# Kernel tuning notes

Hardware: AMD Instinct MI355X
Metric: run time of the kernel (lower is better)

Reference implementation:

```python
import jax, jax.numpy as jnp
import numpy as np

SLOPE = 10.0
NTR = 4.0
DTR = 0.0
DELTA = 3
MARG = 2


def _gt(x):
    return jax.nn.sigmoid(x * SLOPE)


def setup_inputs() -> dict:
    key = jax.random.key(0)
    x = jax.random.uniform(key, (16, 3, 512, 512), dtype=jnp.float32)
    return {"x": x}


def reference(x):
    B, C, H, W = x.shape
    d = DELTA
    # zero-pad H and W by delta (matches the two torch.cat calls)
    im_b = jnp.pad(x, ((0, 0), (0, 0), (d, d), (d, d)))

    roll_hw = lambda s: jnp.roll(im_b, s, axis=(2, 3))
    diff_11 = roll_hw((1, 1)) - im_b
    diff_nn11 = roll_hw((-1, -1)) - im_b
    diff_01 = roll_hw((0, 1)) - im_b
    diff_n01 = roll_hw((0, -1)) - im_b
    diff_10 = roll_hw((1, 0)) - im_b
    diff_n10 = roll_hw((-1, 0)) - im_b
    diff_n11 = roll_hw((-1, 1)) - im_b
    diff_1n1 = roll_hw((1, -1)) - im_b

    # NOTE: the original rolls the diff tensors over dims (1,2) = (channel, H).
    # We reproduce that exactly for faithfulness.
    rl = lambda t, s: jnp.roll(t, s, axis=(1, 2))

    ad_10 = jnp.abs(diff_10)
    ad_10 = ad_10 * _gt(ad_10 - DTR)
    e10a = _gt(ad_10 - jnp.abs(diff_01)) + _gt(ad_10 - jnp.abs(diff_n01)) + _gt(ad_10 - jnp.abs(diff_n10))
    # original repeats the roll(diff_01) term twice
    e10b = (_gt(ad_10 - jnp.abs(rl(diff_01, (1, 0))))
            + _gt(ad_10 - jnp.abs(rl(diff_n01, (1, 0))))
            + _gt(ad_10 - jnp.abs(rl(diff_01, (1, 0)))))
    g10 = _gt(e10a + e10b - NTR)
    e10 = g10 * _gt(diff_10)
    e10n = g10 * _gt(-diff_10)

    ad_01 = jnp.abs(diff_01)
    ad_01 = ad_01 * _gt(ad_10 - DTR)  # original uses ad_10 here (faithful)
    e01a = _gt(ad_01 - jnp.abs(diff_10)) + _gt(ad_01 - jnp.abs(diff_n10)) + _gt(ad_01 - jnp.abs(diff_n01))
    e01b = (_gt(ad_01 - jnp.abs(rl(diff_10, (0, 1))))
            + _gt(ad_01 - jnp.abs(rl(diff_n10, (0, 1))))
            + _gt(ad_01 - jnp.abs(rl(diff_01, (0, 1)))))
    g01 = _gt(e01a + e01b - NTR)
    e01 = g01 * _gt(diff_01)
    e01n = g01 * _gt(diff_01)  # original uses +diff_01 for both (faithful)

    ad_11 = jnp.abs(diff_11)
    ad_11 = ad_11 * _gt(ad_11 - DTR)
    e11a = _gt(ad_11 - jnp.abs(diff_n11)) + _gt(ad_11 - jnp.abs(diff_1n1)) + _gt(ad_11 - jnp.abs(diff_nn11))
    e11b = (_gt(ad_11 - jnp.abs(rl(diff_n11, (1, 1))))
            + _gt(ad_11 - jnp.abs(rl(diff_1n1, (1, 1))))
            + _gt(ad_11 - jnp.abs(rl(diff_11, (1, 1)))))
    g11 = _gt(e11a + e11b - NTR)
    e11 = g11 * _gt(diff_11)
    e11n = g11 * _gt(-diff_11)

    ad_n11 = jnp.abs(diff_n11)
    ad_n11 = ad_n11 * (ad_n11 > DTR).astype(x.dtype)  # hard threshold here (faithful)
    en11a = _gt(ad_n11 - jnp.abs(diff_11)) + _gt(ad_n11 - jnp.abs(diff_1n1)) + _gt(ad_n11 - jnp.abs(diff_nn11))
    en11b = (_gt(ad_n11 - jnp.abs(rl(diff_11, (-1, 1))))
             + _gt(ad_n11 - jnp.abs(rl(diff_n11, (-1, 1))))
             + _gt(ad_n11 - jnp.abs(rl(diff_n11, (-1, 1)))))
    gn11 = _gt(en11a + en11b - NTR)
    en11 = gn11 * _gt(diff_n11)
    en11n = gn11 * _gt(-diff_n11)

    def crop_pad(e):
        # interior crop back to HxW minus margins, zeros elsewhere
        c = e[:, :, d + MARG:d + H - MARG, d + MARG:d + W - MARG]
        return jnp.pad(c, ((0, 0), (0, 0), (MARG, MARG), (MARG, MARG)))

    edges = jnp.stack([crop_pad(e) for e in (e10, e10n, e01, e01n, e11, e11n, en11, en11n)], axis=2)
    # (B, C, 8, H, W) -> (B, 8*C, H, W) in torch's reshape order (C-major)
    return edges.reshape(B, C * 8, H, W)
```

## Files before the change

### kernel.cpp

```cpp
#include <hip/hip_runtime.h>

#define HH 512
#define WW 512

__device__ __forceinline__ float sigm(float t) {
    float e = __builtin_amdgcn_exp2f(t * -14.426950408889634f);
    return __builtin_amdgcn_rcpf(1.0f + e);
}

__global__ __launch_bounds__(256) void edge_kernel(const float* __restrict__ x,
                                                   float* __restrict__ out) {
    const int tx = threadIdx.x & 63;
    const int ty = threadIdx.x >> 6;
    const int w0 = blockIdx.x * 256 + tx * 4;
    const int h  = blockIdx.y * 4 + ty;
    const int b  = blockIdx.z;

    float4* outp = (float4*)(out + (((size_t)(b * 24) * HH + h) * WW + w0));
    const int PL = HH * WW / 4;

    if (h < 2 || h >= HH - 2) {
        const float4 z = make_float4(0.f, 0.f, 0.f, 0.f);
        #pragma unroll
        for (int k = 0; k < 24; ++k) outp[k * PL] = z;
        return;
    }

    float W6[3][4][6];
    const int wl = (w0 == 0) ? 0 : (w0 - 1);
    const int wr = (w0 + 4 >= WW) ? (WW - 1) : (w0 + 4);
    #pragma unroll
    for (int j = 0; j < 3; ++j) {
        const float* rp = x + (((size_t)(b * 3 + j) * HH + (h - 2)) * WW);
        #pragma unroll
        for (int r = 0; r < 4; ++r) {
            const float* row = rp + r * WW;
            const float4 m = *(const float4*)(row + w0);
            W6[j][r][0] = row[wl];
            W6[j][r][1] = m.x; W6[j][r][2] = m.y;
            W6[j][r][3] = m.z; W6[j][r][4] = m.w;
            W6[j][r][5] = row[wr];
        }
    }

    #pragma unroll
    for (int c = 0; c < 3; ++c) {
        const int cm = (c + 2) % 3, cp = (c + 1) % 3;
        float acc[8][4];
        #pragma unroll
        for (int q = 0; q < 4; ++q) {
            const float v = W6[c][2][q + 1], u = W6[c][1][q + 1];
            const float d10   = u              - v;
            const float dn10  = W6[c][3][q+1]  - v;
            const float d01   = W6[c][2][q]    - v;
            const float dn01  = W6[c][2][q+2]  - v;
            const float d11   = W6[c][1][q]    - v;
            const float dnn11 = W6[c][3][q+2]  - v;
            const float dn11  = W6[c][3][q]    - v;
            const float d1n1  = W6[c][1][q+2]  - v;
            const float r_d10 = W6[c][0][q+1]  - u;
            const float r_d01 = W6[c][1][q]    - u;

            const float A01m   = fabsf(W6[cm][2][q]   - W6[cm][2][q+1]);
            const float An01m  = fabsf(W6[cm][2][q+2] - W6[cm][2][q+1]);
            const float rA11m  = fabsf(W6[cm][0][q]   - W6[cm][1][q+1]);
            const float rAn11m = fabsf(W6[cm][2][q]   - W6[cm][1][q+1]);
            const float rA1n1m = fabsf(W6[cm][0][q+2] - W6[cm][1][q+1]);
            const float rA11p  = fabsf(W6[cp][0][q]   - W6[cp][1][q+1]);
            const float rAn11p = fabsf(W6[cp][2][q]   - W6[cp][1][q+1]);

            const float msk = ((w0 + q) >= 2 && (w0 + q) < WW - 2) ? 1.0f : 0.0f;

            const float a10  = fabsf(d10);
            const float ad10 = a10 * sigm(a10);
            const float e10s = sigm(ad10 - fabsf(d01)) + sigm(ad10 - fabsf(dn01))
                             + sigm(ad10 - fabsf(dn10))
                             + 2.0f * sigm(ad10 - A01m)
                             + sigm(ad10 - An01m);
            const float g10 = msk * sigm(e10s - 4.0f);
            const float s10 = sigm(d10);
            acc[0][q] = g10 * s10;
            acc[1][q] = g10 * (1.0f - s10);

            const float ad01 = fabsf(d01) * sigm(ad10);
            const float e01s = 2.0f * sigm(ad01 - a10)
                             + sigm(ad01 - fabsf(dn10)) + sigm(ad01 - fabsf(dn01))
                             + sigm(ad01 - fabsf(r_d10)) + sigm(ad01 - fabsf(r_d01));
            const float g01 = msk * sigm(e01s - 4.0f);
            const float e01 = g01 * sigm(d01);
            acc[2][q] = e01;
            acc[3][q] = e01;

            const float a11  = fabsf(d11);
            const float ad11 = a11 * sigm(a11);
            const float e11s = sigm(ad11 - fabsf(dn11)) + sigm(ad11 - fabsf(d1n1))
                             + sigm(ad11 - fabsf(dnn11))
                             + sigm(ad11 - rAn11m) + sigm(ad11 - rA1n1m)
                             + sigm(ad11 - rA11m);
            const float g11 = msk * sigm(e11s - 4.0f);
            const float s11 = sigm(d11);
            acc[4][q] = g11 * s11;
            acc[5][q] = g11 * (1.0f - s11);

            const float adn11 = fabsf(dn11);
            const float en11s = sigm(adn11 - a11) + sigm(adn11 - fabsf(d1n1))
                              + sigm(adn11 - fabsf(dnn11))
                              + sigm(adn11 - rA11p)
                              + 2.0f * sigm(adn11 - rAn11p);
            const float gn11 = msk * sigm(en11s - 4.0f);
            const float sn11 = sigm(dn11);
            acc[6][q] = gn11 * sn11;
            acc[7][q] = gn11 * (1.0f - sn11);
        }
        #pragma unroll
        for (int k = 0; k < 8; ++k)
            outp[(c * 8 + k) * PL] = make_float4(acc[k][0], acc[k][1], acc[k][2], acc[k][3]);
    }
}

extern "C" void kernel_launch(void* const* d_in, const int* in_sizes, int n_in,
                              void* d_out, int out_size, void* d_ws, size_t ws_size,
                              hipStream_t stream) {
    const float* x = (const float*)d_in[0];
    float* out = (float*)d_out;
    dim3 grid(WW / 256, HH / 4, 16);
    dim3 block(256);
    edge_kernel<<<grid, block, 0, stream>>>(x, out);
}
```

Measured before the change: 452.7 us.

## Split channels across grid, use nontemporal stores and FMA-folded sigmoid args

Each thread now computes one channel instead of all three, tripling the grid and cutting per-thread registers, with a launch-bounds occupancy hint. Output stores become nontemporal to avoid cache pollution on the large write stream. Sigmoid scaling is folded into FMAs to trim ALU work. Neighbour-channel rows are reloaded per block, adding some redundant input reads.

```diff
diff --git a/kernel.cpp b/kernel.cpp
--- a/kernel.cpp
+++ b/kernel.cpp
@@ -2,119 +2,158 @@
 
 #define HH 512
 #define WW 512
+#define KSL 14.426950408889634f
 
-__device__ __forceinline__ float sigm(float t) {
-    float e = __builtin_amdgcn_exp2f(t * -14.426950408889634f);
+typedef float f4 __attribute__((ext_vector_type(4)));
+
+__device__ __forceinline__ float sig_arg(float arg) {
+    float e = __builtin_amdgcn_exp2f(arg);
     return __builtin_amdgcn_rcpf(1.0f + e);
 }
 
-__global__ __launch_bounds__(256) void edge_kernel(const float* __restrict__ x,
-                                                   float* __restrict__ out) {
+__global__ __launch_bounds__(256, 3) void edge_kernel(const float* __restrict__ x,
+                                                      float* __restrict__ out) {
     const int tx = threadIdx.x & 63;
     const int ty = threadIdx.x >> 6;
     const int w0 = blockIdx.x * 256 + tx * 4;
     const int h  = blockIdx.y * 4 + ty;
-    const int b  = blockIdx.z;
+    const int z  = blockIdx.z;
+    const int b  = z / 3;
+    const int c  = z - 3 * b;
 
-    float4* outp = (float4*)(out + (((size_t)(b * 24) * HH + h) * WW + w0));
-    const int PL = HH * WW / 4;
+    float* outp = out + (((size_t)(b * 24 + c * 8) * HH + h) * WW + w0);
+    const int PL = HH * WW;
 
     if (h < 2 || h >= HH - 2) {
-        const float4 z = make_float4(0.f, 0.f, 0.f, 0.f);
+        const f4 zf = {0.f, 0.f, 0.f, 0.f};
         #pragma unroll
-        for (int k = 0; k < 24; ++k) outp[k * PL] = z;
+        for (int k = 0; k < 8; ++k)
+            __builtin_nontemporal_store(zf, (f4*)(outp + k * PL));
         return;
     }
 
-    float W6[3][4][6];
+    const int cm = (c + 2) % 3, cp = (c + 1) % 3;
     const int wl = (w0 == 0) ? 0 : (w0 - 1);
     const int wr = (w0 + 4 >= WW) ? (WW - 1) : (w0 + 4);
-    #pragma unroll
-    for (int j = 0; j < 3; ++j) {
-        const float* rp = x + (((size_t)(b * 3 + j) * HH + (h - 2)) * WW);
+
+    const float* bas = x + (size_t)b * 3 * HH * WW + (size_t)(h - 2) * WW;
+
+    float S[4][6], M[3][6], P[3][6];
+    {
+        const float* rp = bas + (size_t)c * (HH * WW);
         #pragma unroll
         for (int r = 0; r < 4; ++r) {
             const float* row = rp + r * WW;
-            const float4 m = *(const float4*)(row + w0);
-            W6[j][r][0] = row[wl];
-            W6[j][r][1] = m.x; W6[j][r][2] = m.y;
-            W6[j][r][3] = m.z; W6[j][r][4] = m.w;
-            W6[j][r][5] = row[wr];
+            const f4 m = *(const f4*)(row + w0);
+            S[r][1] = m.x; S[r][2] = m.y; S[r][3] = m.z; S[r][4] = m.w;
+            if (r > 0) { S[r][0] = row[wl]; S[r][5] = row[wr]; }
+        }
+    }
+    {
+        const float* rp = bas + (size_t)cm * (HH * WW);
+        #pragma unroll
+        for (int r = 0; r < 3; ++r) {
+            const float* row = rp + r * WW;
+            const f4 m = *(const f4*)(row + w0);
+            M[r][1] = m.x; M[r][2] = m.y; M[r][3] = m.z; M[r][4] = m.w;
+            if (r != 1) { M[r][0] = row[wl]; M[r][5] = row[wr]; }
+        }
+    }
+    {
+        const float* rp = bas + (size_t)cp * (HH * WW);
+        #pragma unroll
+        for (int r = 0; r < 3; ++r) {
+            const float* row = rp + r * WW;
+            const f4 m = *(const f4*)(row + w0);
+            P[r][1] = m.x; P[r][2] = m.y; P[r][3] = m.z; P[r][4] = m.w;
+            if (r != 1) { P[r][0] = row[wl]; }
         }
     }
 
+    float acc[8][4];
     #pragma unroll
-    for (int c = 0; c < 3; ++c) {
-        const int cm = (c + 2) % 3, cp = (c + 1) % 3;
-        float acc[8][4];
-        #pragma unroll
-        for (int q = 0; q < 4; ++q) {
-            const float v = W6[c][2][q + 1], u = W6[c][1][q + 1];
-            const float d10   = u              - v;
-            const float dn10  = W6[c][3][q+1]  - v;
-            const float d01   = W6[c][2][q]    - v;
-            const float dn01  = W6[c][2][q+2]  - v;
-            const float d11   = W6[c][1][q]    - v;
-            const float dnn11 = W6[c][3][q+2]  - v;
-            const float dn11  = W6[c][3][q]    - v;
-            const float d1n1  = W6[c][1][q+2]  - v;
-            const float r_d10 = W6[c][0][q+1]  - u;
-            const float r_d01 = W6[c][1][q]    - u;
+    for (int q = 0; q < 4; ++q) {
+        const float v = S[2][q + 1], u = S[1][q + 1];
+        const float d10   = u           - v;
+        const float dn10  = S[3][q + 1] - v;
+        const float d01   = S[2][q]     - v;
+        const float dn01  = S[2][q + 2] - v;
+        const float d11   = S[1][q]     - v;
+        const float dnn11 = S[3][q + 2] - v;
+        const float dn11  = S[3][q]     - v;
+        const float d1n1  = S[1][q + 2] - v;
+        const float r_d10 = S[0][q + 1] - u;
+        const float r_d01 = S[1][q]     - u;
 
-            const float A01m   = fabsf(W6[cm][2][q]   - W6[cm][2][q+1]);
-            const float An01m  = fabsf(W6[cm][2][q+2] - W6[cm][2][q+1]);
-            const float rA11m  = fabsf(W6[cm][0][q]   - W6[cm][1][q+1]);
-            const float rAn11m = fabsf(W6[cm][2][q]   - W6[cm][1][q+1]);
-            const float rA1n1m = fabsf(W6[cm][0][q+2] - W6[cm][1][q+1]);
-            const float rA11p  = fabsf(W6[cp][0][q]   - W6[cp][1][q+1]);
-            const float rAn11p = fabsf(W6[cp][2][q]   - W6[cp][1][q+1]);
+        const float A01m   = fabsf(M[2][q]     - M[2][q + 1]);
+        const float An01m  = fabsf(M[2][q + 2] - M[2][q + 1]);
+        const float rA11m  = fabsf(M[0][q]     - M[1][q + 1]);
+        const float rAn11m = fabsf(M[2][q]     - M[1][q + 1]);
+        const float rA1n1m = fabsf(M[0][q + 2] - M[1][q + 1]);
+        const float rA11p  = fabsf(P[0][q]     - P[1][q + 1]);
+        const float rAn11p = fabsf(P[2][q]     - P[1][q + 1]);
 
-            const float msk = ((w0 + q) >= 2 && (w0 + q) < WW - 2) ? 1.0f : 0.0f;
+        const float msk = ((w0 + q) >= 2 && (w0 + q) < WW - 2) ? 1.0f : 0.0f;
 
-            const float a10  = fabsf(d10);
-            const float ad10 = a10 * sigm(a10);
-            const float e10s = sigm(ad10 - fabsf(d01)) + sigm(ad10 - fabsf(dn01))
-                             + sigm(ad10 - fabsf(dn10))
-                             + 2.0f * sigm(ad10 - A01m)
-                             + sigm(ad10 - An01m);
-            const float g10 = msk * sigm(e10s - 4.0f);
-            const float s10 = sigm(d10);
-            acc[0][q] = g10 * s10;
-            acc[1][q] = g10 * (1.0f - s10);
+        const float a10  = fabsf(d10);
+        const float sa10 = sig_arg(a10 * -KSL);
+        const float ad10 = a10 * sa10;
+        const float b10  = ad10 * -KSL;
+        const float e10s = sig_arg(fmaf(fabsf(d01),  KSL, b10))
+                         + sig_arg(fmaf(fabsf(dn01), KSL, b10))
+                         + sig_arg(fmaf(fabsf(dn10), KSL, b10))
+                         + 2.0f * sig_arg(fmaf(A01m, KSL, b10))
+                         + sig_arg(fmaf(An01m, KSL, b10));
+        const float g10 = msk * sig_arg(fmaf(e10s, -KSL, 4.0f * KSL));
+        const float s10 = sig_arg(d10 * -KSL);
+        acc[0][q] = g10 * s10;
+        acc[1][q] = fmaf(-s10, g10, g10);
 
-            const float ad01 = fabsf(d01) * sigm(ad10);
-            const float e01s = 2.0f * sigm(ad01 - a10)
-                             + sigm(ad01 - fabsf(dn10)) + sigm(ad01 - fabsf(dn01))
-                             + sigm(ad01 - fabsf(r_d10)) + sigm(ad01 - fabsf(r_d01));
-            const float g01 = msk * sigm(e01s - 4.0f);
-            const float e01 = g01 * sigm(d01);
-            acc[2][q] = e01;
-            acc[3][q] = e01;
+        const float sad10 = sig_arg(b10);
+        const float ad01  = fabsf(d01) * sad10;
+        const float b01   = ad01 * -KSL;
+        const float e01s = 2.0f * sig_arg(fmaf(a10, KSL, b01))
+                         + sig_arg(fmaf(fabsf(dn10),  KSL, b01))
+                         + sig_arg(fmaf(fabsf(dn01),  KSL, b01))
+                         + sig_arg(fmaf(fabsf(r_d10), KSL, b01))
+                         + sig_arg(fmaf(fabsf(r_d01), KSL, b01));
+        const float g01 = msk * sig_arg(fmaf(e01s, -KSL, 4.0f * KSL));
+        const float e01 = g01 * sig_arg(d01 * -KSL);
+        acc[2][q] = e01;
+        acc[3][q] = e01;
 
-            const float a11  = fabsf(d11);
-            const float ad11 = a11 * sigm(a11);
-            const float e11s = sigm(ad11 - fabsf(dn11)) + sigm(ad11 - fabsf(d1n1))
-                             + sigm(ad11 - fabsf(dnn11))
-                             + sigm(ad11 - rAn11m) + sigm(ad11 - rA1n1m)
-                             + sigm(ad11 - rA11m);
-            const float g11 = msk * sigm(e11s - 4.0f);
-            const float s11 = sigm(d11);
-            acc[4][q] = g11 * s11;
-            acc[5][q] = g11 * (1.0f - s11);
+        const float a11  = fabsf(d11);
+        const float sa11 = sig_arg(a11 * -KSL);
+        const float ad11 = a11 * sa11;
+        const float b11  = ad11 * -KSL;
+        const float e11s = sig_arg(fmaf(fabsf(dn11),  KSL, b11))
+                         + sig_arg(fmaf(fabsf(d1n1),  KSL, b11))
+                         + sig_arg(fmaf(fabsf(dnn11), KSL, b11))
+                         + sig_arg(fmaf(rAn11m, KSL, b11))
+                         + sig_arg(fmaf(rA1n1m, KSL, b11))
+                         + sig_arg(fmaf(rA11m,  KSL, b11));
+        const float g11 = msk * sig_arg(fmaf(e11s, -KSL, 4.0f * KSL));
+        const float s11 = sig_arg(d11 * -KSL);
+        acc[4][q] = g11 * s11;
+        acc[5][q] = fmaf(-s11, g11, g11);
 
-            const float adn11 = fabsf(dn11);
-            const float en11s = sigm(adn11 - a11) + sigm(adn11 - fabsf(d1n1))
-                              + sigm(adn11 - fabsf(dnn11))
-                              + sigm(adn11 - rA11p)
-                              + 2.0f * sigm(adn11 - rAn11p);
-            const float gn11 = msk * sigm(en11s - 4.0f);
-            const float sn11 = sigm(dn11);
-            acc[6][q] = gn11 * sn11;
-            acc[7][q] = gn11 * (1.0f - sn11);
-        }
-        #pragma unroll
-        for (int k = 0; k < 8; ++k)
-            outp[(c * 8 + k) * PL] = make_float4(acc[k][0], acc[k][1], acc[k][2], acc[k][3]);
+        const float adn11 = fabsf(dn11);
+        const float bn11  = adn11 * -KSL;
+        const float en11s = sig_arg(fmaf(a11, KSL, bn11))
+                          + sig_arg(fmaf(fabsf(d1n1),  KSL, bn11))
+                          + sig_arg(fmaf(fabsf(dnn11), KSL, bn11))
+                          + sig_arg(fmaf(rA11p, KSL, bn11))
+                          + 2.0f * sig_arg(fmaf(rAn11p, KSL, bn11));
+        const float gn11 = msk * sig_arg(fmaf(en11s, -KSL, 4.0f * KSL));
+        const float sn11 = sig_arg(dn11 * -KSL);
+        acc[6][q] = gn11 * sn11;
+        acc[7][q] = fmaf(-sn11, gn11, gn11);
+    }
+
+    #pragma unroll
+    for (int k = 0; k < 8; ++k) {
+        const f4 o = {acc[k][0], acc[k][1], acc[k][2], acc[k][3]};
+        __builtin_nontemporal_store(o, (f4*)(outp + k * PL));
     }
 }
 
@@ -123,7 +162,7 @@
                               hipStream_t stream) {
     const float* x = (const float*)d_in[0];
     float* out = (float*)d_out;
-    dim3 grid(WW / 256, HH / 4, 16);
+    dim3 grid(WW / 256, HH / 4, 16 * 3);
     dim3 block(256);
     edge_kernel<<<grid, block, 0, stream>>>(x, out);
 }
```

Result: no change. 457.4 us (+1.0%).
